# Optimization experiments

Measured on AMD Instinct MI355X. Metric: run time of the kernel, lower is better.

## Reference

```python
import jax, jax.numpy as jnp
import numpy as np

PRECISION_RATIO = 0.1
ROUTE_THRESH = 0.05

def ternary_quantize(W):
    # TWN-style: delta = 0.7*mean|W|, alpha = mean of kept magnitudes
    delta = 0.7 * jnp.mean(jnp.abs(W))
    mask = (jnp.abs(W) > delta).astype(W.dtype)
    alpha = jnp.sum(jnp.abs(W) * mask) / jnp.maximum(jnp.sum(mask), 1.0)
    return alpha * jnp.sign(W) * mask

def rpb_weight(W, precision_ratio=PRECISION_RATIO):
    # Ternary base + full-precision residual kept for top `precision_ratio` of entries
    Wq = ternary_quantize(W)
    res = W - Wq
    k = max(1, int(precision_ratio * W.size))
    kth = jax.lax.top_k(jnp.abs(res).reshape(-1), k)[0][-1]
    keep = (jnp.abs(res) >= kth).astype(W.dtype)
    return Wq + res * keep

def selective_route(x, threshold=ROUTE_THRESH):
    return x * (jnp.abs(x) >= threshold).astype(x.dtype)

def _lin(x, W, b):
    return x @ W.T + b

def setup_inputs() -> dict:
    key = jax.random.key(0)
    ks = jax.random.split(key, 24)
    B = 8192
    dims = {"vision": 2048, "text": 1024, "audio": 512}
    D = 1024
    T = D * 3  # total_dim = 3072
    s = 0.02
    inp = {
        "x_vision": jax.random.normal(ks[0], (B, dims["vision"]), jnp.float32),
        "x_text": jax.random.normal(ks[1], (B, dims["text"]), jnp.float32),
        "x_audio": jax.random.normal(ks[2], (B, dims["audio"]), jnp.float32),
        "Wv": jax.random.normal(ks[3], (D, dims["vision"]), jnp.float32) * s,
        "bv": jnp.zeros((D,), jnp.float32),
        "Wt": jax.random.normal(ks[4], (D, dims["text"]), jnp.float32) * s,
        "bt": jnp.zeros((D,), jnp.float32),
        "Wa": jax.random.normal(ks[5], (D, dims["audio"]), jnp.float32) * s,
        "ba": jnp.zeros((D,), jnp.float32),
        "Wq1": jax.random.normal(ks[6], (D, T), jnp.float32) * s,
        "bq1": jnp.zeros((D,), jnp.float32),
        "Wq2": jax.random.normal(ks[7], (D, D), jnp.float32) * s,
        "bq2": jnp.zeros((D,), jnp.float32),
        "Wf1": jax.random.normal(ks[8], (D, T), jnp.float32) * s,
        "bf1": jnp.zeros((D,), jnp.float32),
        "Wf2": jax.random.normal(ks[9], (D, D), jnp.float32) * s,
        "bf2": jnp.zeros((D,), jnp.float32),
        "mix_ratio": jnp.asarray(0.75, jnp.float32),
    }
    return inp

def reference(x_vision, x_text, x_audio, Wv, bv, Wt, bt, Wa, ba,
              Wq1, bq1, Wq2, bq2, Wf1, bf1, Wf2, bf2, mix_ratio):
    # per-modality projections then concat in modality order
    pv = _lin(x_vision, Wv, bv)
    pt = _lin(x_text, Wt, bt)
    pa = _lin(x_audio, Wa, ba)
    concat = jnp.concatenate([pv, pt, pa], axis=1)  # [B, 3*D]
    routed = selective_route(concat)
    # quantized (RPB) branch
    h = jax.nn.relu(_lin(routed, rpb_weight(Wq1), bq1))
    out_quant = _lin(h, rpb_weight(Wq2), bq2)
    # full-precision branch
    g = jax.nn.relu(_lin(concat, Wf1, bf1))
    out_full = _lin(g, Wf2, bf2)
    mix = jax.nn.sigmoid(mix_ratio)
    return mix * out_quant + (1.0 - mix) * out_full
```

## Files before the change

### kernel.cpp

```cpp
#include <hip/hip_runtime.h>


typedef _Float16 f16x8 __attribute__((ext_vector_type(8)));
typedef float f32x4 __attribute__((ext_vector_type(4)));

__device__ __forceinline__ unsigned short f16b(float v) {
  union { _Float16 h; unsigned short u; } cv; cv.h = (_Float16)v; return cv.u;
}

__device__ __forceinline__ void load_lds16(const void* g, void* l) {
  __builtin_amdgcn_global_load_lds(
      (const __attribute__((address_space(1))) void*)g,
      (__attribute__((address_space(3))) void*)l, 16, 0, 0);
}

__device__ __forceinline__ float sigmoidf_dev(float x) {
  return 1.0f / (1.0f + expf(-x));
}

#define NB_W1 768
#define NB_TOT 1024

__device__ __forceinline__ float reduce_region_f(const float* part, int lo, int hi,
                                                 float* sbuf) {
  float a = 0.f;
  for (int i = lo + threadIdx.x; i < hi; i += 256) a += part[i];
  sbuf[threadIdx.x] = a; __syncthreads();
  for (int o = 128; o > 0; o >>= 1) {
    if ((int)threadIdx.x < o) sbuf[threadIdx.x] += sbuf[threadIdx.x + o];
    __syncthreads();
  }
  float r = sbuf[0];
  __syncthreads();
  return r;
}

__device__ __forceinline__ float alpha_region(const float* pb, const unsigned* pc,
                                              int lo, int hi, float* sf, unsigned* sc) {
  float a = 0.f; unsigned c = 0;
  for (int i = lo + threadIdx.x; i < hi; i += 256) { a += pb[i]; c += pc[i]; }
  sf[threadIdx.x] = a; sc[threadIdx.x] = c; __syncthreads();
  for (int o = 128; o > 0; o >>= 1) {
    if ((int)threadIdx.x < o) { sf[threadIdx.x] += sf[threadIdx.x + o]; sc[threadIdx.x] += sc[threadIdx.x + o]; }
    __syncthreads();
  }
  float s = sf[0]; float cnt = (float)sc[0];
  __syncthreads();
  if (cnt < 1.f) cnt = 1.f;
  return s / cnt;
}

__device__ __forceinline__ unsigned radix_prefix(const unsigned* __restrict__ hists,
                                                 int w, int nr, unsigned k,
                                                 unsigned* sscan, unsigned* res2) {
  int t = threadIdx.x;
  unsigned prefix = 0, krem = k;
  for (int rr = 0; rr < nr; ++rr) {
    sscan[t] = hists[(rr * 2 + w) * 256 + (255 - t)];
    __syncthreads();
#pragma unroll
    for (int o = 1; o < 256; o <<= 1) {
      unsigned add = (t >= o) ? sscan[t - o] : 0u;
      __syncthreads();
      sscan[t] += add;
      __syncthreads();
    }
    if (sscan[t] >= krem && (t == 0 || sscan[t - 1] < krem)) {
      res2[0] = (unsigned)(255 - t);
      res2[1] = (t == 0) ? 0u : sscan[t - 1];
    }
    __syncthreads();
    prefix |= res2[0] << (24 - 8 * rr);
    krem -= res2[1];
    __syncthreads();
  }
  return prefix;
}

struct Pre1Args {
  const float* src[7];
  unsigned short* dst[7];
  long cum4[8];
  const float* W1; long n41;
  const float* W2; long n42;
  float* part;
  unsigned* hists;
};

__global__ void pre1(Pre1Args a) {
  if (blockIdx.x < 2048) {
    long total = a.cum4[7];
    for (long i = (long)blockIdx.x * 256 + threadIdx.x; i < total;
         i += (long)2048 * 256) {
      int s = 0;
#pragma unroll
      for (int j = 1; j < 7; ++j) s += (i >= a.cum4[j]) ? 1 : 0;
      long off = i - a.cum4[s];
      float4 v = ((const float4*)a.src[s])[off];
      ushort4 o;
      o.x = f16b(v.x); o.y = f16b(v.y); o.z = f16b(v.z); o.w = f16b(v.w);
      ((ushort4*)a.dst[s])[off] = o;
    }
  } else {
    __shared__ float s[256];
    int bid2 = (int)blockIdx.x - 2048;
    if (bid2 < 8) a.hists[bid2 * 256 + threadIdx.x] = 0;
    int w = bid2 < NB_W1 ? 0 : 1;
    const float4* W4 = (const float4*)(w ? a.W2 : a.W1);
    long n4 = w ? a.n42 : a.n41;
    int nb = w ? (NB_TOT - NB_W1) : NB_W1;
    int bid = w ? bid2 - NB_W1 : bid2;
    float acc = 0.f;
    for (long i = (long)bid * 256 + threadIdx.x; i < n4;
         i += (long)nb * 256) {
      float4 v = W4[i];
      acc += fabsf(v.x) + fabsf(v.y) + fabsf(v.z) + fabsf(v.w);
    }
    s[threadIdx.x] = acc; __syncthreads();
    for (int o = 128; o > 0; o >>= 1) {
      if ((int)threadIdx.x < o) s[threadIdx.x] += s[threadIdx.x + o];
      __syncthreads();
    }
    if (threadIdx.x == 0) a.part[bid2] = s[0];
  }
}

__global__ void hist_r(const float* __restrict__ W1, long S1v,
                       const float* __restrict__ W2, long S2v,
                       const float* __restrict__ part,
                       const float* __restrict__ pb, const unsigned* __restrict__ pc,
                       unsigned* __restrict__ hists, int round,
                       unsigned k1, unsigned k2) {
  __shared__ float sf[256]; __shared__ unsigned sc[256];
  __shared__ unsigned h[256]; __shared__ unsigned sscan[256];
  __shared__ unsigned res2[2];
  int t = threadIdx.x;
  int w = blockIdx.x < NB_W1 ? 0 : 1;
  const float* W = w ? W2 : W1;
  long S = w ? S2v : S1v;
  int nb = w ? (NB_TOT - NB_W1) : NB_W1;
  int bid = w ? (int)blockIdx.x - NB_W1 : (int)blockIdx.x;
  int lo = w ? NB_W1 : 0, hi = w ? NB_TOT : NB_W1;
  float tot = reduce_region_f(part, lo, hi, sf);
  float delta = 0.7f * (tot / (float)S);
  float alpha = alpha_region(pb, pc, lo, hi, sf, sc);
  unsigned prefix = radix_prefix(hists, w, round, w ? k2 : k1, sscan, res2);
  h[t] = 0;
  __syncthreads();
  int shift = 24 - 8 * round;
  int hs = shift + 8;
  for (long i = (long)bid * 256 + t; i < S; i += (long)nb * 256) {
    float x = W[i];
    float aw = fabsf(x);
    float wq = (aw > delta) ? copysignf(alpha, x) : 0.0f;
    unsigned ub = __float_as_uint(fabsf(x - wq));
    bool ok = (hs >= 32) || ((ub >> hs) == (prefix >> hs));
    if (ok) atomicAdd(&h[(ub >> shift) & 255u], 1u);
  }
  __syncthreads();
  if (h[t]) atomicAdd(&hists[(round * 2 + w) * 256 + t], h[t]);
}

struct FinArgs {
  const float* Wq1; const float* Wq2; const float* Wf2;
  const float* bq2; const float* bf2; const float* mixp;
  const float* part; const float* pb; const unsigned* pc;
  const unsigned* hists;
  unsigned k1, k2;
  unsigned short* wq1_h;
  unsigned short* w2_h;
  float* b2;
};

__global__ void finalize_weights(FinArgs a) {
  __shared__ float sf[256]; __shared__ unsigned sc[256];
  __shared__ unsigned sscan[256]; __shared__ unsigned res2[2];
  const long S1 = 3145728, S2 = 1048576, D = 1024;
  float tot1 = reduce_region_f(a.part, 0, NB_W1, sf);
  float d1 = 0.7f * (tot1 / (float)S1);
  float tot2 = reduce_region_f(a.part, NB_W1, NB_TOT, sf);
  float d2 = 0.7f * (tot2 / (float)S2);
  float a1 = alpha_region(a.pb, a.pc, 0, NB_W1, sf, sc);
  float a2 = alpha_region(a.pb, a.pc, NB_W1, NB_TOT, sf, sc);
  unsigned kth1 = radix_prefix(a.hists, 0, 4, a.k1, sscan, res2);
  unsigned kth2 = radix_prefix(a.hists, 1, 4, a.k2, sscan, res2);
  float mix = sigmoidf_dev(a.mixp[0]);
  long total = S1 + 2 * S2 + D;
  for (long i = (long)blockIdx.x * blockDim.x + threadIdx.x; i < total;
       i += (long)gridDim.x * blockDim.x) {
    if (i < S1) {
      float x = a.Wq1[i];
      float wq = (fabsf(x) > d1) ? copysignf(a1, x) : 0.0f;
      float res = x - wq;
      float v = wq + ((__float_as_uint(fabsf(res)) >= kth1) ? res : 0.0f);
      a.wq1_h[i] = f16b(v);
    } else if (i < S1 + S2) {
      long j = i - S1; int r = (int)(j >> 10), c = (int)(j & 1023);
      float x = a.Wq2[j];
      float wq = (fabsf(x) > d2) ? copysignf(a2, x) : 0.0f;
      float res = x - wq;
      float v = wq + ((__float_as_uint(fabsf(res)) >= kth2) ? res : 0.0f);
      a.w2_h[(long)r * 2048 + c] = f16b(mix * v);
    } else if (i < S1 + 2 * S2) {
      long j = i - S1 - S2; int r = (int)(j >> 10), c = (int)(j & 1023);
      a.w2_h[(long)r * 2048 + 1024 + c] = f16b((1.0f - mix) * a.Wf2[j]);
    } else {
      long j = i - S1 - 2 * S2;
      a.b2[j] = mix * a.bq2[j] + (1.0f - mix) * a.bf2[j];
    }
  }
}

struct GemmArgs {
  const unsigned short* A0; const unsigned short* A1; const unsigned short* A2;
  const unsigned short* B0; const unsigned short* B1; const unsigned short* B2;
  const float* c0; const float* c1; const float* c2;
  int K0, K1, K2;
  int nrows;
  int ldc;
  int cpsl;
  int nwg;
  unsigned short* o0; unsigned short* o1; float* oF;
  const float* pkW1; long pkS1;
  const float* pkW2; long pkS2;
  const float* pkPart; float* pkPb; unsigned* pkPc;
};

template <int EPI, int BN, bool PK>
__global__ __launch_bounds__(512) void gemm9(GemmArgs g) {
  constexpr int AL = 128 * 32 * 2;
  constexpr int BL = BN * 32 * 2;
  constexpr int BISS = BL / 8192;
  constexpr int NR = BN / 4 / 16;
  __shared__ __align__(16) char sm[2 * AL + 2 * BL];
  const int tid = threadIdx.x;

  if constexpr (PK) {
    if ((int)blockIdx.x >= g.nwg) {
      float* sf = (float*)sm;
      unsigned* sc = (unsigned*)(sm + 2048);
      int bid2 = (int)blockIdx.x - g.nwg;
      int w = bid2 < NB_W1 ? 0 : 1;
      const float* W = w ? g.pkW2 : g.pkW1;
      long S = w ? g.pkS2 : g.pkS1;
      int nb = w ? (NB_TOT - NB_W1) : NB_W1;
      int bid = w ? bid2 - NB_W1 : bid2;
      if (tid < 256) {
        float a = 0.f;
        for (int i = (w ? NB_W1 : 0) + tid; i < (w ? NB_TOT : NB_W1); i += 256)
          a += g.pkPart[i];
        sf[tid] = a;
      }
      __syncthreads();
      for (int o = 128; o > 0; o >>= 1) {
        if (tid < o) sf[tid] += sf[tid + o];
        __syncthreads();
      }
      float delta = 0.7f * (sf[0] / (float)S);
      __syncthreads();
      float a = 0.f; unsigned c = 0;
      for (long i = (long)bid * 512 + tid; i < S; i += (long)nb * 512) {
        float aw = fabsf(W[i]);
        if (aw > delta) { a += aw; ++c; }
      }
      sf[tid] = a; sc[tid] = c; __syncthreads();
      for (int o = 256; o > 0; o >>= 1) {
        if (tid < o) { sf[tid] += sf[tid + o]; sc[tid] += sc[tid + o]; }
        __syncthreads();
      }
      if (tid == 0) { g.pkPb[bid2] = sf[0]; g.pkPc[bid2] = sc[0]; }
      return;
    }
  }

  const int wid = tid >> 6;
  const int lane = tid & 63;
  const int wm = wid >> 2, wn = wid & 3;

  const int nwg = g.nwg;
  const int id = (blockIdx.x & 7) * (nwg >> 3) + (blockIdx.x >> 3);
  const int ncols = nwg / g.nrows;
  const int c = id % ncols, r = id / ncols;
  const int sel = c >> g.cpsl, lc = c & ((1 << g.cpsl) - 1);

  const unsigned short* A = sel == 0 ? g.A0 : (sel == 1 ? g.A1 : g.A2);
  const unsigned short* Bw = sel == 0 ? g.B0 : (sel == 1 ? g.B1 : g.B2);
  const float* bias = sel == 0 ? g.c0 : (sel == 1 ? g.c1 : g.c2);
  const int K = sel == 0 ? g.K0 : (sel == 1 ? g.K1 : g.K2);
  const long brow = (long)r * 128;
  const int bRowB = lc * BN;

  f32x4 acc[4][NR];
#pragma unroll
  for (int i = 0; i < 4; ++i)
#pragma unroll
    for (int j = 0; j < NR; ++j)
#pragma unroll
      for (int e = 0; e < 4; ++e) acc[i][j][e] = 0.f;

  const int oA = tid * 16;
  const unsigned short* aSrc = A + (brow + (oA >> 6)) * (long)K + ((oA & 63) >> 1);
  const unsigned short* bSrc[BISS];
#pragma unroll
  for (int j = 0; j < BISS; ++j) {
    int o = j * 8192 + tid * 16;
    bSrc[j] = Bw + (long)(bRowB + (o >> 6)) * K + ((o & 63) >> 1);
  }

  auto STAGE = [&](int buf, int k0) {
    load_lds16(aSrc + k0, sm + (size_t)buf * AL + wid * 1024);
#pragma unroll
    for (int j = 0; j < BISS; ++j)
      load_lds16(bSrc[j] + k0, sm + 2 * AL + (size_t)buf * BL + j * 8192 + wid * 1024);
  };

  const int kb = (lane >> 4) * 16;
  auto COMPUTE = [&](int buf) {
    const char* lAp = sm + (size_t)buf * AL;
    const char* lBp = sm + 2 * AL + (size_t)buf * BL;
    f16x8 a[4], b[NR];
#pragma unroll
    for (int m = 0; m < 4; ++m)
      a[m] = *(const f16x8*)(lAp + (wm * 64 + m * 16 + (lane & 15)) * 64 + kb);
#pragma unroll
    for (int n = 0; n < NR; ++n)
      b[n] = *(const f16x8*)(lBp + (wn * (BN / 4) + n * 16 + (lane & 15)) * 64 + kb);
#pragma unroll
    for (int m = 0; m < 4; ++m)
#pragma unroll
      for (int n = 0; n < NR; ++n)
        acc[m][n] = __builtin_amdgcn_mfma_f32_16x16x32_f16(a[m], b[n], acc[m][n], 0, 0, 0);
  };

  const int NT = K >> 5;
  STAGE(0, 0);
  __syncthreads();
  int cur = 0;
  for (int t = 0; t < NT - 1; ++t) {
    STAGE(cur ^ 1, (t + 1) << 5);
    COMPUTE(cur);
    __syncthreads();
    cur ^= 1;
  }
  COMPUTE(cur);

  const int cb = c * BN + wn * (BN / 4);
  const int rb = r * 128 + wm * 64;
  const int bcol0 = bRowB + wn * (BN / 4);
#pragma unroll
  for (int i = 0; i < 4; ++i) {
    int r0 = rb + i * 16 + ((lane >> 4) << 2);
#pragma unroll
    for (int j = 0; j < NR; ++j) {
      int ccol = cb + j * 16 + (lane & 15);
      float bb = bias[bcol0 + j * 16 + (lane & 15)];
#pragma unroll
      for (int e = 0; e < 4; ++e) {
        float v = acc[i][j][e] + bb;
        long idx = (long)(r0 + e) * g.ldc + ccol;
        if constexpr (EPI == 0) {
          g.o0[idx] = f16b(v);
          g.o1[idx] = f16b(fabsf(v) >= 0.05f ? v : 0.0f);
        } else if constexpr (EPI == 1) {
          g.o0[idx] = f16b(fmaxf(v, 0.0f));
        } else {
          g.oF[idx] = v;
        }
      }
    }
  }
}

extern "C" void kernel_launch(void* const* d_in, const int* in_sizes, int n_in,
                              void* d_out, int out_size, void* d_ws, size_t ws_size,
                              hipStream_t stream) {
  const float* xv = (const float*)d_in[0];
  const float* xt = (const float*)d_in[1];
  const float* xa = (const float*)d_in[2];
  const float* Wv = (const float*)d_in[3];
  const float* bv = (const float*)d_in[4];
  const float* Wt = (const float*)d_in[5];
  const float* bt = (const float*)d_in[6];
  const float* Wa = (const float*)d_in[7];
  const float* ba = (const float*)d_in[8];
  const float* Wq1 = (const float*)d_in[9];
  const float* bq1 = (const float*)d_in[10];
  const float* Wq2 = (const float*)d_in[11];
  const float* bq2 = (const float*)d_in[12];
  const float* Wf1 = (const float*)d_in[13];
  const float* bf1 = (const float*)d_in[14];
  const float* Wf2 = (const float*)d_in[15];
  const float* bf2 = (const float*)d_in[16];
  const float* mixp = (const float*)d_in[17];

  const int B = 8192, D = 1024, T = 3072;
  const int Kv = 2048, Kt = 1024, Ka = 512;
  const long S1 = (long)D * T, S2 = (long)D * D;

  char* w = (char*)d_ws;
  auto alloc = [&](size_t bytes) -> char* {
    char* p = w; w += (bytes + 255) & ~(size_t)255; return p;
  };
  unsigned short* xv_h = (unsigned short*)alloc((size_t)B * Kv * 2);
  unsigned short* xt_h = (unsigned short*)alloc((size_t)B * Kt * 2);
  unsigned short* xa_h = (unsigned short*)alloc((size_t)B * Ka * 2);
  unsigned short* wv_h = (unsigned short*)alloc((size_t)D * Kv * 2);
  unsigned short* wt_h = (unsigned short*)alloc((size_t)D * Kt * 2);
  unsigned short* wa_h = (unsigned short*)alloc((size_t)D * Ka * 2);
  unsigned short* wq1_h = (unsigned short*)alloc((size_t)D * T * 2);
  unsigned short* wf1_h = (unsigned short*)alloc((size_t)D * T * 2);
  unsigned short* w2_h = (unsigned short*)alloc((size_t)D * 2048 * 2);
  unsigned short* concat_h = (unsigned short*)alloc((size_t)B * T * 2);
  unsigned short* routed_h = (unsigned short*)alloc((size_t)B * T * 2);
  unsigned short* a2_h = (unsigned short*)alloc((size_t)B * 2048 * 2);
  float* b2 = (float*)alloc(D * 4);
  float* part = (float*)alloc(1024 * 4);
  float* pb = (float*)alloc(1024 * 4);
  unsigned* pc = (unsigned*)alloc(1024 * 4);
  unsigned* hists = (unsigned*)alloc(4 * 2 * 256 * 4);

  const unsigned k1 = (unsigned)(S1 / 10), k2 = (unsigned)(S2 / 10);

  Pre1Args pa;
  pa.src[0] = xv;  pa.dst[0] = xv_h;
  pa.src[1] = xt;  pa.dst[1] = xt_h;
  pa.src[2] = xa;  pa.dst[2] = xa_h;
  pa.src[3] = Wv;  pa.dst[3] = wv_h;
  pa.src[4] = Wt;  pa.dst[4] = wt_h;
  pa.src[5] = Wa;  pa.dst[5] = wa_h;
  pa.src[6] = Wf1; pa.dst[6] = wf1_h;
  long n4s[7] = {(long)B * Kv / 4, (long)B * Kt / 4, (long)B * Ka / 4,
                 (long)D * Kv / 4, (long)D * Kt / 4, (long)D * Ka / 4, S1 / 4};
  pa.cum4[0] = 0;
  for (int i = 0; i < 7; ++i) pa.cum4[i + 1] = pa.cum4[i] + n4s[i];
  pa.W1 = Wq1; pa.n41 = S1 / 4;
  pa.W2 = Wq2; pa.n42 = S2 / 4;
  pa.part = part; pa.hists = hists;
  pre1<<<3072, 256, 0, stream>>>(pa);

  GemmArgs gp;
  gp.A0 = xv_h; gp.A1 = xt_h; gp.A2 = xa_h;
  gp.B0 = wv_h; gp.B1 = wt_h; gp.B2 = wa_h;
  gp.c0 = bv; gp.c1 = bt; gp.c2 = ba;
  gp.K0 = Kv; gp.K1 = Kt; gp.K2 = Ka;
  gp.nrows = B / 128; gp.ldc = T; gp.cpsl = 2; gp.nwg = 12 * (B / 128);
  gp.o0 = concat_h; gp.o1 = routed_h; gp.oF = nullptr;
  gp.pkW1 = Wq1; gp.pkS1 = S1;
  gp.pkW2 = Wq2; gp.pkS2 = S2;
  gp.pkPart = part; gp.pkPb = pb; gp.pkPc = pc;
  gemm9<0, 256, true><<<gp.nwg + NB_TOT, 512, 0, stream>>>(gp);

  for (int rr = 0; rr < 4; ++rr)
    hist_r<<<NB_TOT, 256, 0, stream>>>(Wq1, S1, Wq2, S2, part, pb, pc,
                                       hists, rr, k1, k2);

  FinArgs fw;
  fw.Wq1 = Wq1; fw.Wq2 = Wq2; fw.Wf2 = Wf2;
  fw.bq2 = bq2; fw.bf2 = bf2; fw.mixp = mixp;
  fw.part = part; fw.pb = pb; fw.pc = pc; fw.hists = hists;
  fw.k1 = k1; fw.k2 = k2;
  fw.wq1_h = wq1_h; fw.w2_h = w2_h; fw.b2 = b2;
  finalize_weights<<<1024, 256, 0, stream>>>(fw);

  GemmArgs gh;
  gh.A0 = routed_h; gh.A1 = concat_h; gh.A2 = routed_h;
  gh.B0 = wq1_h; gh.B1 = wf1_h; gh.B2 = wq1_h;
  gh.c0 = bq1; gh.c1 = bf1; gh.c2 = bq1;
  gh.K0 = T; gh.K1 = T; gh.K2 = T;
  gh.nrows = B / 128; gh.ldc = 2048; gh.cpsl = 2; gh.nwg = 8 * (B / 128);
  gh.o0 = a2_h; gh.o1 = nullptr; gh.oF = nullptr;
  gemm9<1, 256, false><<<gh.nwg, 512, 0, stream>>>(gh);

  GemmArgs gf;
  gf.A0 = a2_h; gf.A1 = a2_h; gf.A2 = a2_h;
  gf.B0 = w2_h; gf.B1 = w2_h; gf.B2 = w2_h;
  gf.c0 = b2; gf.c1 = b2; gf.c2 = b2;
  gf.K0 = 2048; gf.K1 = 2048; gf.K2 = 2048;
  gf.nrows = B / 128; gf.ldc = D; gf.cpsl = 3; gf.nwg = 8 * (B / 128);
  gf.o0 = nullptr; gf.o1 = nullptr; gf.oF = (float*)d_out;
  gemm9<2, 128, false><<<gf.nwg, 512, 0, stream>>>(gf);
}
```

Before: 393.5 us.

## Triple-buffer GEMM LDS pipeline with split-phase MFMA scheduling and setprio

Replaces the double-buffered K loop of the fp16 MFMA GEMM with a three-slot LDS ring that keeps two tiles in flight. Each tile is split into two phases: a few LDS loads, then issuing part of the next stage's global-to-LDS loads, then a burst of MFMAs at raised wave priority, with fine-grained vmcnt waits instead of full __syncthreads. The aim is to hide global load latency and interleave LDS reads with matrix work. In exchange it uses 1.5x the LDS per block, which can lower occupancy, and depends on manual waitcnt counts that must match the number of issued loads. It also adds a second launch_bounds argument.

```diff
diff --git a/kernel.cpp b/kernel.cpp
--- a/kernel.cpp
+++ b/kernel.cpp
@@ -227,12 +227,14 @@
 };
 
 template <int EPI, int BN, bool PK>
-__global__ __launch_bounds__(512) void gemm9(GemmArgs g) {
+__global__ __launch_bounds__(512, 4) void gemmP(GemmArgs g) {
   constexpr int AL = 128 * 32 * 2;
   constexpr int BL = BN * 32 * 2;
+  constexpr int TL = AL + BL;
   constexpr int BISS = BL / 8192;
-  constexpr int NR = BN / 4 / 16;
-  __shared__ __align__(16) char sm[2 * AL + 2 * BL];
+  constexpr int NR = BN / 64;
+  constexpr int WN = BN / 4;
+  __shared__ __align__(16) char sm[3 * TL];
   const int tid = threadIdx.x;
 
   if constexpr (PK) {
@@ -307,46 +309,85 @@
     bSrc[j] = Bw + (long)(bRowB + (o >> 6)) * K + ((o & 63) >> 1);
   }
 
-  auto STAGE = [&](int buf, int k0) {
-    load_lds16(aSrc + k0, sm + (size_t)buf * AL + wid * 1024);
-#pragma unroll
-    for (int j = 0; j < BISS; ++j)
-      load_lds16(bSrc[j] + k0, sm + 2 * AL + (size_t)buf * BL + j * 8192 + wid * 1024);
+  auto STAGE_A = [&](int slot, int k0) {
+    load_lds16(aSrc + k0, sm + (size_t)slot * TL + wid * 1024);
   };
+  auto STAGE_B = [&](int slot, int k0, int j) {
+    load_lds16(bSrc[j] + k0, sm + (size_t)slot * TL + AL + j * 8192 + wid * 1024);
+  };
 
   const int kb = (lane >> 4) * 16;
-  auto COMPUTE = [&](int buf) {
-    const char* lAp = sm + (size_t)buf * AL;
-    const char* lBp = sm + 2 * AL + (size_t)buf * BL;
-    f16x8 a[4], b[NR];
-#pragma unroll
-    for (int m = 0; m < 4; ++m)
-      a[m] = *(const f16x8*)(lAp + (wm * 64 + m * 16 + (lane & 15)) * 64 + kb);
+  auto DS_A = [&](const char* lAp, int m) -> f16x8 {
+    return *(const f16x8*)(lAp + (wm * 64 + m * 16 + (lane & 15)) * 64 + kb);
+  };
+
+  auto TILE = [&](int sc2, int ss, int kst, bool doStage, bool cntWait) {
+    const char* lAp = sm + (size_t)sc2 * TL;
+    const char* lBp = lAp + AL;
+    f16x8 b[NR];
 #pragma unroll
     for (int n = 0; n < NR; ++n)
-      b[n] = *(const f16x8*)(lBp + (wn * (BN / 4) + n * 16 + (lane & 15)) * 64 + kb);
-#pragma unroll
-    for (int m = 0; m < 4; ++m)
-#pragma unroll
-      for (int n = 0; n < NR; ++n)
-        acc[m][n] = __builtin_amdgcn_mfma_f32_16x16x32_f16(a[m], b[n], acc[m][n], 0, 0, 0);
+      b[n] = *(const f16x8*)(lBp + (wn * WN + n * 16 + (lane & 15)) * 64 + kb);
+    f16x8 a0 = DS_A(lAp, 0), a1 = DS_A(lAp, 1);
+    if (doStage) { STAGE_A(ss, kst); STAGE_B(ss, kst, 0); }
+    __builtin_amdgcn_s_barrier();
+    asm volatile("s_waitcnt lgkmcnt(0)" ::: "memory");
+    __builtin_amdgcn_sched_barrier(0);
+    __builtin_amdgcn_s_setprio(1);
+#pragma unroll
+    for (int n = 0; n < NR; ++n)
+      acc[0][n] = __builtin_amdgcn_mfma_f32_16x16x32_f16(a0, b[n], acc[0][n], 0, 0, 0);
+#pragma unroll
+    for (int n = 0; n < NR; ++n)
+      acc[1][n] = __builtin_amdgcn_mfma_f32_16x16x32_f16(a1, b[n], acc[1][n], 0, 0, 0);
+    __builtin_amdgcn_s_setprio(0);
+    __builtin_amdgcn_s_barrier();
+    f16x8 a2 = DS_A(lAp, 2), a3 = DS_A(lAp, 3);
+    if (doStage && BISS == 2) STAGE_B(ss, kst, 1);
+    __builtin_amdgcn_s_barrier();
+    asm volatile("s_waitcnt lgkmcnt(0)" ::: "memory");
+    __builtin_amdgcn_sched_barrier(0);
+    __builtin_amdgcn_s_setprio(1);
+#pragma unroll
+    for (int n = 0; n < NR; ++n)
+      acc[2][n] = __builtin_amdgcn_mfma_f32_16x16x32_f16(a2, b[n], acc[2][n], 0, 0, 0);
+#pragma unroll
+    for (int n = 0; n < NR; ++n)
+      acc[3][n] = __builtin_amdgcn_mfma_f32_16x16x32_f16(a3, b[n], acc[3][n], 0, 0, 0);
+    __builtin_amdgcn_s_setprio(0);
+    if (cntWait) {
+      if constexpr (BISS == 2) asm volatile("s_waitcnt vmcnt(3)" ::: "memory");
+      else                     asm volatile("s_waitcnt vmcnt(2)" ::: "memory");
+    } else {
+      asm volatile("s_waitcnt vmcnt(0)" ::: "memory");
+    }
+    __builtin_amdgcn_s_barrier();
   };
 
   const int NT = K >> 5;
-  STAGE(0, 0);
-  __syncthreads();
-  int cur = 0;
-  for (int t = 0; t < NT - 1; ++t) {
-    STAGE(cur ^ 1, (t + 1) << 5);
-    COMPUTE(cur);
-    __syncthreads();
-    cur ^= 1;
-  }
-  COMPUTE(cur);
-
-  const int cb = c * BN + wn * (BN / 4);
+  STAGE_A(0, 0);
+#pragma unroll
+  for (int j = 0; j < BISS; ++j) STAGE_B(0, 0, j);
+  STAGE_A(1, 32);
+#pragma unroll
+  for (int j = 0; j < BISS; ++j) STAGE_B(1, 32, j);
+  if constexpr (BISS == 2) asm volatile("s_waitcnt vmcnt(3)" ::: "memory");
+  else                     asm volatile("s_waitcnt vmcnt(2)" ::: "memory");
+  __builtin_amdgcn_s_barrier();
+
+  int s0 = 0;
+  for (int t = 0; t < NT; t += 2) {
+    const int s1v = (s0 + 1 == 3) ? 0 : s0 + 1;
+    const int s2v = (s1v + 1 == 3) ? 0 : s1v + 1;
+    const bool st2 = (t + 2 < NT);
+    TILE(s0, s2v, (t + 2) << 5, st2, st2);
+    TILE(s1v, s0, (t + 3) << 5, st2, st2);
+    s0 = s2v;
+  }
+
+  const int cb = c * BN + wn * WN;
   const int rb = r * 128 + wm * 64;
-  const int bcol0 = bRowB + wn * (BN / 4);
+  const int bcol0 = bRowB + wn * WN;
 #pragma unroll
   for (int i = 0; i < 4; ++i) {
     int r0 = rb + i * 16 + ((lane >> 4) << 2);
@@ -448,7 +489,7 @@
   gp.pkW1 = Wq1; gp.pkS1 = S1;
   gp.pkW2 = Wq2; gp.pkS2 = S2;
   gp.pkPart = part; gp.pkPb = pb; gp.pkPc = pc;
-  gemm9<0, 256, true><<<gp.nwg + NB_TOT, 512, 0, stream>>>(gp);
+  gemmP<0, 256, true><<<gp.nwg + NB_TOT, 512, 0, stream>>>(gp);
 
   for (int rr = 0; rr < 4; ++rr)
     hist_r<<<NB_TOT, 256, 0, stream>>>(Wq1, S1, Wq2, S2, part, pb, pc,
@@ -469,7 +510,7 @@
   gh.K0 = T; gh.K1 = T; gh.K2 = T;
   gh.nrows = B / 128; gh.ldc = 2048; gh.cpsl = 2; gh.nwg = 8 * (B / 128);
   gh.o0 = a2_h; gh.o1 = nullptr; gh.oF = nullptr;
-  gemm9<1, 256, false><<<gh.nwg, 512, 0, stream>>>(gh);
+  gemmP<1, 256, false><<<gh.nwg, 512, 0, stream>>>(gh);
 
   GemmArgs gf;
   gf.A0 = a2_h; gf.A1 = a2_h; gf.A2 = a2_h;
@@ -478,5 +519,5 @@
   gf.K0 = 2048; gf.K1 = 2048; gf.K2 = 2048;
   gf.nrows = B / 128; gf.ldc = D; gf.cpsl = 3; gf.nwg = 8 * (B / 128);
   gf.o0 = nullptr; gf.o1 = nullptr; gf.oF = (float*)d_out;
-  gemm9<2, 128, false><<<gf.nwg, 512, 0, stream>>>(gf);
-}
+  gemmP<2, 128, false><<<gf.nwg, 512, 0, stream>>>(gf);
+}
```

Result: no change. 395.4 us (+0.5%).

## Use 256x256 tiles with BK=64 and explicit LDS pipeline for big GEMMs

Applied to the files above, without the earlier changes.

Replaces the 128xBN GEMM used for the projection and hidden layers with a 256x256 tile, K-step of 64 and 128KB of dynamic LDS. Loads are two stages ahead, with manual waitcnt, barriers and setprio to overlap MFMA with global-to-LDS copies. The final GEMM moves to its own specialized 128x128 kernel. The larger tile raises arithmetic intensity and halves the tile count, at the cost of fewer workgroups, heavy register pressure (128 accumulators per thread) and possible LDS bank conflicts from the new layout.

```diff
diff --git a/kernel.cpp b/kernel.cpp
--- a/kernel.cpp
+++ b/kernel.cpp
@@ -226,13 +226,9 @@
   const float* pkPart; float* pkPb; unsigned* pkPc;
 };
 
-template <int EPI, int BN, bool PK>
-__global__ __launch_bounds__(512) void gemm9(GemmArgs g) {
-  constexpr int AL = 128 * 32 * 2;
-  constexpr int BL = BN * 32 * 2;
-  constexpr int BISS = BL / 8192;
-  constexpr int NR = BN / 4 / 16;
-  __shared__ __align__(16) char sm[2 * AL + 2 * BL];
+template <int EPI, bool PK>
+__global__ __launch_bounds__(512, 2) void gemmBig(GemmArgs g) {
+  extern __shared__ __align__(16) char sm[];
   const int tid = threadIdx.x;
 
   if constexpr (PK) {
@@ -287,48 +283,185 @@
   const unsigned short* Bw = sel == 0 ? g.B0 : (sel == 1 ? g.B1 : g.B2);
   const float* bias = sel == 0 ? g.c0 : (sel == 1 ? g.c1 : g.c2);
   const int K = sel == 0 ? g.K0 : (sel == 1 ? g.K1 : g.K2);
+  const long brow = (long)r * 256;
+  const int bRowB = lc * 256;
+
+  f32x4 acc[8][4];
+#pragma unroll
+  for (int i = 0; i < 8; ++i)
+#pragma unroll
+    for (int j = 0; j < 4; ++j)
+#pragma unroll
+      for (int e = 0; e < 4; ++e) acc[i][j][e] = 0.f;
+
+  const int rr = tid & 127;
+  const int kc0 = tid >> 7;
+  const unsigned short* srcQ[4][2];
+#pragma unroll
+  for (int q = 0; q < 2; ++q)
+#pragma unroll
+    for (int i = 0; i < 2; ++i) {
+      srcQ[q][i]     = A  + (brow + q * 128 + rr) * (long)K + (i * 4 + kc0) * 8;
+      srcQ[q + 2][i] = Bw + (long)(bRowB + q * 128 + rr) * K + (i * 4 + kc0) * 8;
+    }
+
+  auto STAGE = [&](int buf, int t) {
+    char* base = sm + (size_t)buf * 65536;
+    const int koff = t * 64;
+#pragma unroll
+    for (int q = 0; q < 4; ++q)
+#pragma unroll
+      for (int i = 0; i < 2; ++i)
+        load_lds16(srcQ[q][i] + koff, base + q * 16384 + i * 8192 + wid * 1024);
+  };
+
+  const int l15 = lane & 15, l4 = lane >> 4;
+  const int aQ = wm * 16384;
+  const int bQ = (2 + (wn >> 1)) * 16384;
+  const int bR0 = (wn & 1) * 64;
+
+  auto RD = [&](int buf, int qoff, int kk, int rowl) -> f16x8 {
+    return *(const f16x8*)(sm + (size_t)buf * 65536 + qoff +
+                           (kk * 4 + l4) * 2048 + rowl * 16);
+  };
+
+  const int NT = K >> 6;
+  STAGE(0, 0);
+  STAGE(1, 1);
+  asm volatile("s_waitcnt vmcnt(8)" ::: "memory");
+  __builtin_amdgcn_s_barrier();
+  __builtin_amdgcn_sched_barrier(0);
+
+  for (int t = 0; t < NT; ++t) {
+    const int buf = t & 1;
+    f16x8 b[2][4], a[2][4];
+#pragma unroll
+    for (int kk = 0; kk < 2; ++kk)
+#pragma unroll
+      for (int n = 0; n < 4; ++n)
+        b[kk][n] = RD(buf, bQ, kk, bR0 + n * 16 + l15);
+#pragma unroll
+    for (int kk = 0; kk < 2; ++kk)
+#pragma unroll
+      for (int m = 0; m < 4; ++m)
+        a[kk][m] = RD(buf, aQ, kk, m * 16 + l15);
+    asm volatile("s_waitcnt lgkmcnt(0)" ::: "memory");
+    __builtin_amdgcn_sched_barrier(0);
+    __builtin_amdgcn_s_setprio(1);
+#pragma unroll
+    for (int kk = 0; kk < 2; ++kk)
+#pragma unroll
+      for (int m = 0; m < 4; ++m)
+#pragma unroll
+        for (int n = 0; n < 4; ++n)
+          acc[m][n] = __builtin_amdgcn_mfma_f32_16x16x32_f16(a[kk][m], b[kk][n], acc[m][n], 0, 0, 0);
+    __builtin_amdgcn_s_setprio(0);
+#pragma unroll
+    for (int kk = 0; kk < 2; ++kk)
+#pragma unroll
+      for (int m = 0; m < 4; ++m)
+        a[kk][m] = RD(buf, aQ, kk, 64 + m * 16 + l15);
+    asm volatile("s_waitcnt lgkmcnt(0)" ::: "memory");
+    __builtin_amdgcn_sched_barrier(0);
+    __builtin_amdgcn_s_barrier();
+    __builtin_amdgcn_sched_barrier(0);
+    if (t + 2 < NT) STAGE(buf, t + 2);
+    __builtin_amdgcn_s_setprio(1);
+#pragma unroll
+    for (int kk = 0; kk < 2; ++kk)
+#pragma unroll
+      for (int m = 0; m < 4; ++m)
+#pragma unroll
+        for (int n = 0; n < 4; ++n)
+          acc[4 + m][n] = __builtin_amdgcn_mfma_f32_16x16x32_f16(a[kk][m], b[kk][n], acc[4 + m][n], 0, 0, 0);
+    __builtin_amdgcn_s_setprio(0);
+    if (t + 2 < NT) asm volatile("s_waitcnt vmcnt(8)" ::: "memory");
+    else            asm volatile("s_waitcnt vmcnt(0)" ::: "memory");
+    __builtin_amdgcn_s_barrier();
+    __builtin_amdgcn_sched_barrier(0);
+  }
+
+  const int cb = c * 256 + wn * 64;
+  const int rb = r * 256 + wm * 128;
+  const int bcol0 = bRowB + wn * 64;
+#pragma unroll
+  for (int qr = 0; qr < 2; ++qr)
+#pragma unroll
+    for (int m = 0; m < 4; ++m) {
+      int r0 = rb + qr * 64 + m * 16 + (l4 << 2);
+#pragma unroll
+      for (int n = 0; n < 4; ++n) {
+        int ccol = cb + n * 16 + l15;
+        float bb = bias[bcol0 + n * 16 + l15];
+#pragma unroll
+        for (int e = 0; e < 4; ++e) {
+          float v = acc[qr * 4 + m][n][e] + bb;
+          long idx = (long)(r0 + e) * g.ldc + ccol;
+          if constexpr (EPI == 0) {
+            g.o0[idx] = f16b(v);
+            g.o1[idx] = f16b(fabsf(v) >= 0.05f ? v : 0.0f);
+          } else {
+            g.o0[idx] = f16b(fmaxf(v, 0.0f));
+          }
+        }
+      }
+    }
+}
+
+__global__ __launch_bounds__(512) void gemmFin(GemmArgs g) {
+  constexpr int AL = 128 * 32 * 2;
+  constexpr int BL = 128 * 32 * 2;
+  __shared__ __align__(16) char sm[2 * AL + 2 * BL];
+  const int tid = threadIdx.x;
+  const int wid = tid >> 6;
+  const int lane = tid & 63;
+  const int wm = wid >> 2, wn = wid & 3;
+
+  const int nwg = g.nwg;
+  const int id = (blockIdx.x & 7) * (nwg >> 3) + (blockIdx.x >> 3);
+  const int ncols = nwg / g.nrows;
+  const int c = id % ncols, r = id / ncols;
+  const int lc = c;
+
+  const unsigned short* A = g.A0;
+  const unsigned short* Bw = g.B0;
+  const float* bias = g.c0;
+  const int K = g.K0;
   const long brow = (long)r * 128;
-  const int bRowB = lc * BN;
-
-  f32x4 acc[4][NR];
+  const int bRowB = lc * 128;
+
+  f32x4 acc[4][2];
 #pragma unroll
   for (int i = 0; i < 4; ++i)
 #pragma unroll
-    for (int j = 0; j < NR; ++j)
+    for (int j = 0; j < 2; ++j)
 #pragma unroll
       for (int e = 0; e < 4; ++e) acc[i][j][e] = 0.f;
 
   const int oA = tid * 16;
   const unsigned short* aSrc = A + (brow + (oA >> 6)) * (long)K + ((oA & 63) >> 1);
-  const unsigned short* bSrc[BISS];
-#pragma unroll
-  for (int j = 0; j < BISS; ++j) {
-    int o = j * 8192 + tid * 16;
-    bSrc[j] = Bw + (long)(bRowB + (o >> 6)) * K + ((o & 63) >> 1);
-  }
+  const unsigned short* bSrc = Bw + (long)(bRowB + (oA >> 6)) * K + ((oA & 63) >> 1);
 
   auto STAGE = [&](int buf, int k0) {
     load_lds16(aSrc + k0, sm + (size_t)buf * AL + wid * 1024);
-#pragma unroll
-    for (int j = 0; j < BISS; ++j)
-      load_lds16(bSrc[j] + k0, sm + 2 * AL + (size_t)buf * BL + j * 8192 + wid * 1024);
+    load_lds16(bSrc + k0, sm + 2 * AL + (size_t)buf * BL + wid * 1024);
   };
 
   const int kb = (lane >> 4) * 16;
   auto COMPUTE = [&](int buf) {
     const char* lAp = sm + (size_t)buf * AL;
     const char* lBp = sm + 2 * AL + (size_t)buf * BL;
-    f16x8 a[4], b[NR];
+    f16x8 a[4], b[2];
 #pragma unroll
     for (int m = 0; m < 4; ++m)
       a[m] = *(const f16x8*)(lAp + (wm * 64 + m * 16 + (lane & 15)) * 64 + kb);
 #pragma unroll
-    for (int n = 0; n < NR; ++n)
-      b[n] = *(const f16x8*)(lBp + (wn * (BN / 4) + n * 16 + (lane & 15)) * 64 + kb);
+    for (int n = 0; n < 2; ++n)
+      b[n] = *(const f16x8*)(lBp + (wn * 32 + n * 16 + (lane & 15)) * 64 + kb);
 #pragma unroll
     for (int m = 0; m < 4; ++m)
 #pragma unroll
-      for (int n = 0; n < NR; ++n)
+      for (int n = 0; n < 2; ++n)
         acc[m][n] = __builtin_amdgcn_mfma_f32_16x16x32_f16(a[m], b[n], acc[m][n], 0, 0, 0);
   };
 
@@ -344,28 +477,20 @@
   }
   COMPUTE(cur);
 
-  const int cb = c * BN + wn * (BN / 4);
+  const int cb = c * 128 + wn * 32;
   const int rb = r * 128 + wm * 64;
-  const int bcol0 = bRowB + wn * (BN / 4);
+  const int bcol0 = bRowB + wn * 32;
 #pragma unroll
   for (int i = 0; i < 4; ++i) {
     int r0 = rb + i * 16 + ((lane >> 4) << 2);
 #pragma unroll
-    for (int j = 0; j < NR; ++j) {
+    for (int j = 0; j < 2; ++j) {
       int ccol = cb + j * 16 + (lane & 15);
       float bb = bias[bcol0 + j * 16 + (lane & 15)];
 #pragma unroll
       for (int e = 0; e < 4; ++e) {
         float v = acc[i][j][e] + bb;
-        long idx = (long)(r0 + e) * g.ldc + ccol;
-        if constexpr (EPI == 0) {
-          g.o0[idx] = f16b(v);
-          g.o1[idx] = f16b(fabsf(v) >= 0.05f ? v : 0.0f);
-        } else if constexpr (EPI == 1) {
-          g.o0[idx] = f16b(fmaxf(v, 0.0f));
-        } else {
-          g.oF[idx] = v;
-        }
+        g.oF[(long)(r0 + e) * g.ldc + ccol] = v;
       }
     }
   }
@@ -421,6 +546,11 @@
 
   const unsigned k1 = (unsigned)(S1 / 10), k2 = (unsigned)(S2 / 10);
 
+  (void)hipFuncSetAttribute((const void*)&gemmBig<0, true>,
+                            hipFuncAttributeMaxDynamicSharedMemorySize, 131072);
+  (void)hipFuncSetAttribute((const void*)&gemmBig<1, false>,
+                            hipFuncAttributeMaxDynamicSharedMemorySize, 131072);
+
   Pre1Args pa;
   pa.src[0] = xv;  pa.dst[0] = xv_h;
   pa.src[1] = xt;  pa.dst[1] = xt_h;
@@ -443,12 +573,12 @@
   gp.B0 = wv_h; gp.B1 = wt_h; gp.B2 = wa_h;
   gp.c0 = bv; gp.c1 = bt; gp.c2 = ba;
   gp.K0 = Kv; gp.K1 = Kt; gp.K2 = Ka;
-  gp.nrows = B / 128; gp.ldc = T; gp.cpsl = 2; gp.nwg = 12 * (B / 128);
+  gp.nrows = B / 256; gp.ldc = T; gp.cpsl = 2; gp.nwg = 12 * (B / 256);
   gp.o0 = concat_h; gp.o1 = routed_h; gp.oF = nullptr;
   gp.pkW1 = Wq1; gp.pkS1 = S1;
   gp.pkW2 = Wq2; gp.pkS2 = S2;
   gp.pkPart = part; gp.pkPb = pb; gp.pkPc = pc;
-  gemm9<0, 256, true><<<gp.nwg + NB_TOT, 512, 0, stream>>>(gp);
+  gemmBig<0, true><<<gp.nwg + NB_TOT, 512, 131072, stream>>>(gp);
 
   for (int rr = 0; rr < 4; ++rr)
     hist_r<<<NB_TOT, 256, 0, stream>>>(Wq1, S1, Wq2, S2, part, pb, pc,
@@ -467,9 +597,9 @@
   gh.B0 = wq1_h; gh.B1 = wf1_h; gh.B2 = wq1_h;
   gh.c0 = bq1; gh.c1 = bf1; gh.c2 = bq1;
   gh.K0 = T; gh.K1 = T; gh.K2 = T;
-  gh.nrows = B / 128; gh.ldc = 2048; gh.cpsl = 2; gh.nwg = 8 * (B / 128);
+  gh.nrows = B / 256; gh.ldc = 2048; gh.cpsl = 2; gh.nwg = 8 * (B / 256);
   gh.o0 = a2_h; gh.o1 = nullptr; gh.oF = nullptr;
-  gemm9<1, 256, false><<<gh.nwg, 512, 0, stream>>>(gh);
+  gemmBig<1, false><<<gh.nwg, 512, 131072, stream>>>(gh);
 
   GemmArgs gf;
   gf.A0 = a2_h; gf.A1 = a2_h; gf.A2 = a2_h;
@@ -478,5 +608,5 @@
   gf.K0 = 2048; gf.K1 = 2048; gf.K2 = 2048;
   gf.nrows = B / 128; gf.ldc = D; gf.cpsl = 3; gf.nwg = 8 * (B / 128);
   gf.o0 = nullptr; gf.o1 = nullptr; gf.oF = (float*)d_out;
-  gemm9<2, 128, false><<<gf.nwg, 512, 0, stream>>>(gf);
-}
+  gemmFin<<<gf.nwg, 512, 0, stream>>>(gf);
+}
```

Result: slower. 457.4 us (+16.3%).

## Fuse radix histogram rounds and weight finalize into one cooperative kernel

Applied to the files above, without the earlier changes.

Replaces four separate histogram-round launches plus the finalize launch with a single cooperative kernel that uses grid-wide syncs between radix rounds. This removes four kernel launch boundaries and their launch gaps on the serial quantization path. A fallback to the old multi-launch path is kept if the cooperative launch fails. Grid.sync cost and the need for all 1024 blocks to be co-resident are the tradeoffs.

```diff
diff --git a/kernel.cpp b/kernel.cpp
--- a/kernel.cpp
+++ b/kernel.cpp
@@ -1,4 +1,7 @@
 #include <hip/hip_runtime.h>
+#include <hip/hip_cooperative_groups.h>
+
+namespace cg = cooperative_groups;
 
 
 typedef _Float16 f16x8 __attribute__((ext_vector_type(8)));
@@ -125,65 +128,21 @@
   }
 }
 
-__global__ void hist_r(const float* __restrict__ W1, long S1v,
-                       const float* __restrict__ W2, long S2v,
-                       const float* __restrict__ part,
-                       const float* __restrict__ pb, const unsigned* __restrict__ pc,
-                       unsigned* __restrict__ hists, int round,
-                       unsigned k1, unsigned k2) {
-  __shared__ float sf[256]; __shared__ unsigned sc[256];
-  __shared__ unsigned h[256]; __shared__ unsigned sscan[256];
-  __shared__ unsigned res2[2];
-  int t = threadIdx.x;
-  int w = blockIdx.x < NB_W1 ? 0 : 1;
-  const float* W = w ? W2 : W1;
-  long S = w ? S2v : S1v;
-  int nb = w ? (NB_TOT - NB_W1) : NB_W1;
-  int bid = w ? (int)blockIdx.x - NB_W1 : (int)blockIdx.x;
-  int lo = w ? NB_W1 : 0, hi = w ? NB_TOT : NB_W1;
-  float tot = reduce_region_f(part, lo, hi, sf);
-  float delta = 0.7f * (tot / (float)S);
-  float alpha = alpha_region(pb, pc, lo, hi, sf, sc);
-  unsigned prefix = radix_prefix(hists, w, round, w ? k2 : k1, sscan, res2);
-  h[t] = 0;
-  __syncthreads();
-  int shift = 24 - 8 * round;
-  int hs = shift + 8;
-  for (long i = (long)bid * 256 + t; i < S; i += (long)nb * 256) {
-    float x = W[i];
-    float aw = fabsf(x);
-    float wq = (aw > delta) ? copysignf(alpha, x) : 0.0f;
-    unsigned ub = __float_as_uint(fabsf(x - wq));
-    bool ok = (hs >= 32) || ((ub >> hs) == (prefix >> hs));
-    if (ok) atomicAdd(&h[(ub >> shift) & 255u], 1u);
-  }
-  __syncthreads();
-  if (h[t]) atomicAdd(&hists[(round * 2 + w) * 256 + t], h[t]);
-}
-
 struct FinArgs {
   const float* Wq1; const float* Wq2; const float* Wf2;
   const float* bq2; const float* bf2; const float* mixp;
   const float* part; const float* pb; const unsigned* pc;
-  const unsigned* hists;
+  unsigned* hists;
   unsigned k1, k2;
   unsigned short* wq1_h;
   unsigned short* w2_h;
   float* b2;
 };
 
-__global__ void finalize_weights(FinArgs a) {
-  __shared__ float sf[256]; __shared__ unsigned sc[256];
-  __shared__ unsigned sscan[256]; __shared__ unsigned res2[2];
+__device__ __forceinline__ void finalize_body(const FinArgs& a,
+                                              float d1, float a1, unsigned kth1,
+                                              float d2, float a2, unsigned kth2) {
   const long S1 = 3145728, S2 = 1048576, D = 1024;
-  float tot1 = reduce_region_f(a.part, 0, NB_W1, sf);
-  float d1 = 0.7f * (tot1 / (float)S1);
-  float tot2 = reduce_region_f(a.part, NB_W1, NB_TOT, sf);
-  float d2 = 0.7f * (tot2 / (float)S2);
-  float a1 = alpha_region(a.pb, a.pc, 0, NB_W1, sf, sc);
-  float a2 = alpha_region(a.pb, a.pc, NB_W1, NB_TOT, sf, sc);
-  unsigned kth1 = radix_prefix(a.hists, 0, 4, a.k1, sscan, res2);
-  unsigned kth2 = radix_prefix(a.hists, 1, 4, a.k2, sscan, res2);
   float mix = sigmoidf_dev(a.mixp[0]);
   long total = S1 + 2 * S2 + D;
   for (long i = (long)blockIdx.x * blockDim.x + threadIdx.x; i < total;
@@ -209,6 +168,99 @@
       a.b2[j] = mix * a.bq2[j] + (1.0f - mix) * a.bf2[j];
     }
   }
+}
+
+__global__ void rpb_fused(FinArgs a) {
+  cg::grid_group grid = cg::this_grid();
+  __shared__ float sf[256]; __shared__ unsigned sc[256];
+  __shared__ unsigned h[256]; __shared__ unsigned sscan[256];
+  __shared__ unsigned res2[2];
+  const long S1 = 3145728, S2 = 1048576;
+  int t = threadIdx.x;
+  int w = blockIdx.x < NB_W1 ? 0 : 1;
+  const float* W = w ? a.Wq2 : a.Wq1;
+  long S = w ? S2 : S1;
+  int nb = w ? (NB_TOT - NB_W1) : NB_W1;
+  int bid = w ? (int)blockIdx.x - NB_W1 : (int)blockIdx.x;
+  int lo = w ? NB_W1 : 0, hi = w ? NB_TOT : NB_W1;
+  float tot = reduce_region_f(a.part, lo, hi, sf);
+  float delta = 0.7f * (tot / (float)S);
+  float alpha = alpha_region(a.pb, a.pc, lo, hi, sf, sc);
+  unsigned kw = w ? a.k2 : a.k1;
+  for (int round = 0; round < 4; ++round) {
+    unsigned prefix = radix_prefix(a.hists, w, round, kw, sscan, res2);
+    h[t] = 0;
+    __syncthreads();
+    int shift = 24 - 8 * round;
+    int hs = shift + 8;
+    for (long i = (long)bid * 256 + t; i < S; i += (long)nb * 256) {
+      float x = W[i];
+      float aw = fabsf(x);
+      float wq = (aw > delta) ? copysignf(alpha, x) : 0.0f;
+      unsigned ub = __float_as_uint(fabsf(x - wq));
+      bool ok = (hs >= 32) || ((ub >> hs) == (prefix >> hs));
+      if (ok) atomicAdd(&h[(ub >> shift) & 255u], 1u);
+    }
+    __syncthreads();
+    if (h[t]) atomicAdd(&a.hists[(round * 2 + w) * 256 + t], h[t]);
+    grid.sync();
+  }
+  float tot1 = reduce_region_f(a.part, 0, NB_W1, sf);
+  float d1 = 0.7f * (tot1 / (float)S1);
+  float tot2 = reduce_region_f(a.part, NB_W1, NB_TOT, sf);
+  float d2 = 0.7f * (tot2 / (float)S2);
+  float a1 = alpha_region(a.pb, a.pc, 0, NB_W1, sf, sc);
+  float a2 = alpha_region(a.pb, a.pc, NB_W1, NB_TOT, sf, sc);
+  unsigned kth1 = radix_prefix(a.hists, 0, 4, a.k1, sscan, res2);
+  unsigned kth2 = radix_prefix(a.hists, 1, 4, a.k2, sscan, res2);
+  finalize_body(a, d1, a1, kth1, d2, a2, kth2);
+}
+
+__global__ void hist_r(FinArgs a, int round) {
+  __shared__ float sf[256]; __shared__ unsigned sc[256];
+  __shared__ unsigned h[256]; __shared__ unsigned sscan[256];
+  __shared__ unsigned res2[2];
+  const long S1 = 3145728, S2 = 1048576;
+  int t = threadIdx.x;
+  int w = blockIdx.x < NB_W1 ? 0 : 1;
+  const float* W = w ? a.Wq2 : a.Wq1;
+  long S = w ? S2 : S1;
+  int nb = w ? (NB_TOT - NB_W1) : NB_W1;
+  int bid = w ? (int)blockIdx.x - NB_W1 : (int)blockIdx.x;
+  int lo = w ? NB_W1 : 0, hi = w ? NB_TOT : NB_W1;
+  float tot = reduce_region_f(a.part, lo, hi, sf);
+  float delta = 0.7f * (tot / (float)S);
+  float alpha = alpha_region(a.pb, a.pc, lo, hi, sf, sc);
+  unsigned prefix = radix_prefix(a.hists, w, round, w ? a.k2 : a.k1, sscan, res2);
+  h[t] = 0;
+  __syncthreads();
+  int shift = 24 - 8 * round;
+  int hs = shift + 8;
+  for (long i = (long)bid * 256 + t; i < S; i += (long)nb * 256) {
+    float x = W[i];
+    float aw = fabsf(x);
+    float wq = (aw > delta) ? copysignf(alpha, x) : 0.0f;
+    unsigned ub = __float_as_uint(fabsf(x - wq));
+    bool ok = (hs >= 32) || ((ub >> hs) == (prefix >> hs));
+    if (ok) atomicAdd(&h[(ub >> shift) & 255u], 1u);
+  }
+  __syncthreads();
+  if (h[t]) atomicAdd(&a.hists[(round * 2 + w) * 256 + t], h[t]);
+}
+
+__global__ void finalize_weights(FinArgs a) {
+  __shared__ float sf[256]; __shared__ unsigned sc[256];
+  __shared__ unsigned sscan[256]; __shared__ unsigned res2[2];
+  const long S1 = 3145728, S2 = 1048576;
+  float tot1 = reduce_region_f(a.part, 0, NB_W1, sf);
+  float d1 = 0.7f * (tot1 / (float)S1);
+  float tot2 = reduce_region_f(a.part, NB_W1, NB_TOT, sf);
+  float d2 = 0.7f * (tot2 / (float)S2);
+  float a1 = alpha_region(a.pb, a.pc, 0, NB_W1, sf, sc);
+  float a2 = alpha_region(a.pb, a.pc, NB_W1, NB_TOT, sf, sc);
+  unsigned kth1 = radix_prefix(a.hists, 0, 4, a.k1, sscan, res2);
+  unsigned kth2 = radix_prefix(a.hists, 1, 4, a.k2, sscan, res2);
+  finalize_body(a, d1, a1, kth1, d2, a2, kth2);
 }
 
 struct GemmArgs {
@@ -450,17 +502,23 @@
   gp.pkPart = part; gp.pkPb = pb; gp.pkPc = pc;
   gemm9<0, 256, true><<<gp.nwg + NB_TOT, 512, 0, stream>>>(gp);
 
-  for (int rr = 0; rr < 4; ++rr)
-    hist_r<<<NB_TOT, 256, 0, stream>>>(Wq1, S1, Wq2, S2, part, pb, pc,
-                                       hists, rr, k1, k2);
-
   FinArgs fw;
   fw.Wq1 = Wq1; fw.Wq2 = Wq2; fw.Wf2 = Wf2;
   fw.bq2 = bq2; fw.bf2 = bf2; fw.mixp = mixp;
   fw.part = part; fw.pb = pb; fw.pc = pc; fw.hists = hists;
   fw.k1 = k1; fw.k2 = k2;
   fw.wq1_h = wq1_h; fw.w2_h = w2_h; fw.b2 = b2;
-  finalize_weights<<<1024, 256, 0, stream>>>(fw);
+  {
+    void* kargs[] = { (void*)&fw };
+    hipError_t ce = hipLaunchCooperativeKernel((void*)rpb_fused, dim3(NB_TOT),
+                                               dim3(256), kargs, 0, stream);
+    if (ce != hipSuccess) {
+      (void)hipGetLastError();
+      for (int rr = 0; rr < 4; ++rr)
+        hist_r<<<NB_TOT, 256, 0, stream>>>(fw, rr);
+      finalize_weights<<<1024, 256, 0, stream>>>(fw);
+    }
+  }
 
   GemmArgs gh;
   gh.A0 = routed_h; gh.A1 = concat_h; gh.A2 = routed_h;
```

New measurement: 802.6 us. 104% more time.
